# Kernel optimization log

Measured on AMD Instinct MI355X. Metric: run time of the kernel, lower is better.

The kernel has to match this reference:

```python
import jax, jax.numpy as jnp
import numpy as np
import math

N, K, M = 4, 3, 3
OUTC, INC = 64, 64

def _valid_combos():
    combos = []
    for n in range(1, N + 1):
        for k in range(K):
            for m in range(-M, M + 1):
                if abs(m) <= k and k < n:
                    combos.append((n, k, m))
    return combos

COMBOS = _valid_combos()  # 23 (n,k,m) triples, static


def _assoc_laguerre(k, a, x):
    # L_k^a(x) = sum_{i=0}^k (-1)^i C(k+a, k-i) x^i / i!  (static small degree)
    out = jnp.zeros_like(x)
    for i in range(k + 1):
        c = ((-1) ** i) * math.comb(k + a, k - i) / math.factorial(i)
        out = out + jnp.asarray(c, x.dtype) * x ** i
    return out


def _assoc_legendre(l, m, ct, st):
    # P_l^m(cos t) with Condon-Shortley phase; ct=cos t, st=sin t >= 0
    if m > 0:
        dfact = math.prod(range(1, 2 * m, 2))  # (2m-1)!!
        pmm = jnp.asarray(((-1) ** m) * dfact, ct.dtype) * st ** m
    else:
        pmm = jnp.ones_like(ct)
    if l == m:
        return pmm
    pmmp1 = ct * (2 * m + 1) * pmm
    if l == m + 1:
        return pmmp1
    for ll in range(m + 2, l + 1):
        pll = ((2 * ll - 1) * ct * pmmp1 - (ll + m - 1) * pmm) / (ll - m)
        pmm, pmmp1 = pmmp1, pll
    return pmmp1


def _hwfr(n, l, m, r, ct, st, phi):
    # real hydrogen-like wavefunction psi_{n,l,m}(r,theta,phi), a0 = 1
    rho = 2.0 * r / n
    norm_r = math.sqrt((2.0 / n) ** 3 * math.factorial(n - l - 1) / (2 * n * math.factorial(n + l)))
    R = norm_r * jnp.exp(-0.5 * rho) * rho ** l * _assoc_laguerre(n - l - 1, 2 * l + 1, rho)
    am = abs(m)
    Klm = math.sqrt((2 * l + 1) / (4 * math.pi) * math.factorial(l - am) / math.factorial(l + am))
    P = _assoc_legendre(l, am, ct, st)
    if m > 0:
        Y = math.sqrt(2.0) * Klm * jnp.cos(am * phi) * P
    elif m < 0:
        Y = math.sqrt(2.0) * Klm * jnp.sin(am * phi) * P
    else:
        Y = Klm * P
    return R * Y


def setup_inputs() -> dict:
    key = jax.random.key(0)
    k1, k2 = jax.random.split(key)
    position = jax.random.normal(k1, (8, 4096, 3), dtype=jnp.float32)
    coefficients = jax.random.normal(k2, (OUTC, INC, len(COMBOS)), dtype=jnp.float32)
    return {"position": position, "coefficients": coefficients}


def reference(position, coefficients):
    x, y, z = position[..., 0], position[..., 1], position[..., 2]
    r = jnp.sqrt(x * x + y * y + z * z) + 1e-12
    ct = z / r
    st = jnp.sqrt(jnp.clip(1.0 - ct * ct, 0.0, None))
    phi = jnp.arctan2(y, x)
    # (B, P, n_basis) -- loop over the small static basis set, not data dims
    poly = jnp.stack([_hwfr(n, l, m, r, ct, st, phi) for (n, l, m) in COMBOS], axis=-1)
    # einsum 'ijk, mnk -> mnij' as in the torch module -> (OutC, InC, B, P)
    return jnp.einsum('ijk,mnk->mnij', poly, coefficients)
```

## Files before the change

### kernel.cpp

```cpp
#include <hip/hip_runtime.h>
#include <math.h>

#define NPTS  32768
#define NPAIR 4096
#define NC    23
#define TPB   256
#define PPT   4
#define PTS_PER_BLOCK (TPB * PPT)
#define PT    64
#define NCP   24

namespace cgen {
constexpr double PI = 3.14159265358979323846264338327950288;
constexpr double fact(int n) { double r = 1; for (int i = 2; i <= n; ++i) r *= i; return r; }
constexpr double comb(int n, int k) { double r = 1; for (int i = 0; i < k; ++i) r = r * (n - i) / (i + 1); return r; }
constexpr double csqrt(double x) { double g = x > 1 ? x : 1.0; for (int i = 0; i < 100; ++i) g = 0.5 * (g + x / g); return g; }

struct Tables {
  int n[NC]; int l[NC]; int m[NC];
  double pref[NC];
  double lag[NC][4];
};
constexpr Tables gen() {
  Tables t{};
  int idx = 0;
  for (int n = 1; n <= 4; ++n)
    for (int k = 0; k < 3; ++k)
      for (int m = -3; m <= 3; ++m) {
        int am = m < 0 ? -m : m;
        if (!(am <= k && k < n)) continue;
        t.n[idx] = n; t.l[idx] = k; t.m[idx] = m;
        double norm_r = csqrt((2.0 / n) * (2.0 / n) * (2.0 / n) * fact(n - k - 1) / (2.0 * n * fact(n + k)));
        double Klm = csqrt((2.0 * k + 1.0) / (4.0 * PI) * fact(k - am) / fact(k + am));
        t.pref[idx] = norm_r * Klm * (m != 0 ? csqrt(2.0) : 1.0);
        int kk = n - k - 1, a = 2 * k + 1;
        for (int i = 0; i < 4; ++i) t.lag[idx][i] = 0.0;
        for (int i = 0; i <= kk; ++i)
          t.lag[idx][i] = ((i & 1) ? -1.0 : 1.0) * comb(kk + a, kk - i) / fact(i);
        ++idx;
      }
  return t;
}
constexpr Tables T = gen();
}

__global__ __launch_bounds__(TPB)
void dcconv_poly_einsum(const float* __restrict__ pos,
                        const float* __restrict__ coef,
                        float* __restrict__ out) {
  __shared__ __align__(16) float lc[PT * NCP];

  const int tid   = threadIdx.x;
  const int pt0   = blockIdx.x * PTS_PER_BLOCK + tid * PPT;
  const int pair0 = blockIdx.y * PT;

  {
    const float* __restrict__ cb = coef + (size_t)pair0 * NC;
#pragma unroll
    for (int i = tid; i < PT * NC; i += TPB) {
      const int row = i / NC;
      const int col = i - row * NC;
      lc[row * NCP + col] = cb[i];
    }
    if (tid < PT) lc[tid * NCP + NC] = 0.0f;
  }

  const float4* __restrict__ pv = reinterpret_cast<const float4*>(pos + (size_t)pt0 * 3);
  const float4 q0 = pv[0], q1 = pv[1], q2 = pv[2];

  float p0[NC], p1[NC], p2[NC], p3[NC];

  auto evalpt = [&](float x, float y, float z, float (&pc)[NC]) {
    const float r   = sqrtf(x * x + y * y + z * z) + 1e-12f;
    const float ct  = z / r;
    const float st2 = fmaxf(1.0f - ct * ct, 0.0f);
    const float st  = sqrtf(st2);
    const float phi = atan2f(y, x);
    float sp, cp;
    sincosf(phi, &sp, &cp);
    const float c2p = cp * cp - sp * sp;
    const float s2p = 2.0f * sp * cp;

    float rho[5]; rho[0] = 0.0f; rho[1] = 2.0f * r; rho[2] = r; rho[3] = (2.0f / 3.0f) * r; rho[4] = 0.5f * r;
    float en[5];  en[0] = 0.0f;
    en[1] = expf(-r); en[2] = expf(-0.5f * r); en[3] = expf(-(1.0f / 3.0f) * r); en[4] = expf(-0.25f * r);

    float P[3][3] = {};
    P[0][0] = 1.0f;
    P[1][0] = ct;                    P[1][1] = -st;
    P[2][0] = 1.5f * ct * ct - 0.5f; P[2][1] = -3.0f * ct * st; P[2][2] = 3.0f * st2;

    float trig[5]; trig[0] = s2p; trig[1] = sp; trig[2] = 1.0f; trig[3] = cp; trig[4] = c2p;

#pragma unroll
    for (int c = 0; c < NC; ++c) {
      const int n = cgen::T.n[c], l = cgen::T.l[c], m = cgen::T.m[c];
      const int am = m < 0 ? -m : m;
      const float rh = rho[n];
      const float L = (float)cgen::T.lag[c][0]
                    + rh * ((float)cgen::T.lag[c][1]
                    + rh * ((float)cgen::T.lag[c][2]
                    + rh *  (float)cgen::T.lag[c][3]));
      const float rl = (l == 0) ? 1.0f : ((l == 1) ? rh : rh * rh);
      pc[c] = (float)cgen::T.pref[c] * en[n] * rl * L * P[l][am] * trig[m + 2];
    }
  };

  evalpt(q0.x, q0.y, q0.z, p0);
  evalpt(q0.w, q1.x, q1.y, p1);
  evalpt(q1.z, q1.w, q2.x, p2);
  evalpt(q2.y, q2.z, q2.w, p3);

  __syncthreads();

  const float4* __restrict__ lrow = reinterpret_cast<const float4*>(lc);
  float* __restrict__ optr = out + (size_t)pair0 * NPTS + pt0;

#define G4(CV, B)                                                                      \
  a0 = fmaf(CV.x, p0[(B)+0], a0); a1 = fmaf(CV.x, p1[(B)+0], a1);                       \
  a2 = fmaf(CV.x, p2[(B)+0], a2); a3 = fmaf(CV.x, p3[(B)+0], a3);                       \
  a0 = fmaf(CV.y, p0[(B)+1], a0); a1 = fmaf(CV.y, p1[(B)+1], a1);                       \
  a2 = fmaf(CV.y, p2[(B)+1], a2); a3 = fmaf(CV.y, p3[(B)+1], a3);                       \
  a0 = fmaf(CV.z, p0[(B)+2], a0); a1 = fmaf(CV.z, p1[(B)+2], a1);                       \
  a2 = fmaf(CV.z, p2[(B)+2], a2); a3 = fmaf(CV.z, p3[(B)+2], a3);                       \
  a0 = fmaf(CV.w, p0[(B)+3], a0); a1 = fmaf(CV.w, p1[(B)+3], a1);                       \
  a2 = fmaf(CV.w, p2[(B)+3], a2); a3 = fmaf(CV.w, p3[(B)+3], a3);

#define G3(CV, B)                                                                      \
  a0 = fmaf(CV.x, p0[(B)+0], a0); a1 = fmaf(CV.x, p1[(B)+0], a1);                       \
  a2 = fmaf(CV.x, p2[(B)+0], a2); a3 = fmaf(CV.x, p3[(B)+0], a3);                       \
  a0 = fmaf(CV.y, p0[(B)+1], a0); a1 = fmaf(CV.y, p1[(B)+1], a1);                       \
  a2 = fmaf(CV.y, p2[(B)+1], a2); a3 = fmaf(CV.y, p3[(B)+1], a3);                       \
  a0 = fmaf(CV.z, p0[(B)+2], a0); a1 = fmaf(CV.z, p1[(B)+2], a1);                       \
  a2 = fmaf(CV.z, p2[(B)+2], a2); a3 = fmaf(CV.z, p3[(B)+2], a3);

#pragma unroll 2
  for (int j = 0; j < PT; ++j) {
    const float4 c0 = lrow[0], c1 = lrow[1], c2 = lrow[2],
                 c3 = lrow[3], c4 = lrow[4], c5 = lrow[5];
    lrow += 6;

    float a0 = 0.0f, a1 = 0.0f, a2 = 0.0f, a3 = 0.0f;
    G4(c0, 0) G4(c1, 4) G4(c2, 8) G4(c3, 12) G4(c4, 16) G3(c5, 20)

    *reinterpret_cast<float4*>(optr) = make_float4(a0, a1, a2, a3);
    optr += NPTS;
  }
#undef G4
#undef G3
}

extern "C" void kernel_launch(void* const* d_in, const int* in_sizes, int n_in,
                              void* d_out, int out_size, void* d_ws, size_t ws_size,
                              hipStream_t stream) {
  const float* pos  = (const float*)d_in[0];
  const float* coef = (const float*)d_in[1];
  float* out = (float*)d_out;

  dim3 grid(NPTS / PTS_PER_BLOCK, NPAIR / PT);
  dim3 block(TPB);
  hipLaunchKernelGGL(dcconv_poly_einsum, grid, block, 0, stream, pos, coef, out);
}
```

Baseline: 546.7 us.

## Halve points per thread, raise occupancy, simplify trig/exp, prefetch coefficient rows

Result: no change. 540.1 us (-1.2%).

```diff
diff --git a/kernel.cpp b/kernel.cpp
--- a/kernel.cpp
+++ b/kernel.cpp
@@ -5,7 +5,7 @@
 #define NPAIR 4096
 #define NC    23
 #define TPB   256
-#define PPT   4
+#define PPT   2
 #define PTS_PER_BLOCK (TPB * PPT)
 #define PT    64
 #define NCP   24
@@ -44,11 +44,11 @@
 constexpr Tables T = gen();
 }
 
-__global__ __launch_bounds__(TPB)
+__global__ __launch_bounds__(TPB, 4)
 void dcconv_poly_einsum(const float* __restrict__ pos,
                         const float* __restrict__ coef,
                         float* __restrict__ out) {
-  __shared__ __align__(16) float lc[PT * NCP];
+  __shared__ __align__(16) float lc[(PT + 1) * NCP];
 
   const int tid   = threadIdx.x;
   const int pt0   = blockIdx.x * PTS_PER_BLOCK + tid * PPT;
@@ -62,28 +62,31 @@
       const int col = i - row * NC;
       lc[row * NCP + col] = cb[i];
     }
-    if (tid < PT) lc[tid * NCP + NC] = 0.0f;
   }
 
-  const float4* __restrict__ pv = reinterpret_cast<const float4*>(pos + (size_t)pt0 * 3);
-  const float4 q0 = pv[0], q1 = pv[1], q2 = pv[2];
+  const float2* __restrict__ pv = reinterpret_cast<const float2*>(pos + (size_t)pt0 * 3);
+  const float2 f0 = pv[0], f1 = pv[1], f2 = pv[2];
 
-  float p0[NC], p1[NC], p2[NC], p3[NC];
+  float p0[NC], p1[NC];
 
   auto evalpt = [&](float x, float y, float z, float (&pc)[NC]) {
-    const float r   = sqrtf(x * x + y * y + z * z) + 1e-12f;
-    const float ct  = z / r;
-    const float st2 = fmaxf(1.0f - ct * ct, 0.0f);
-    const float st  = sqrtf(st2);
-    const float phi = atan2f(y, x);
-    float sp, cp;
-    sincosf(phi, &sp, &cp);
-    const float c2p = cp * cp - sp * sp;
-    const float s2p = 2.0f * sp * cp;
+    const float rxy2 = x * x + y * y;
+    const float r    = sqrtf(rxy2 + z * z) + 1e-12f;
+    const float ct   = z / r;
+    const float st   = sqrtf(rxy2) / r;
+    const float st2  = st * st;
+    const float invq = rsqrtf(fmaxf(rxy2, 1e-30f));
+    const float cp   = x * invq;
+    const float sp   = y * invq;
+    const float c2p  = (cp - sp) * (cp + sp);
+    const float s2p  = 2.0f * sp * cp;
 
     float rho[5]; rho[0] = 0.0f; rho[1] = 2.0f * r; rho[2] = r; rho[3] = (2.0f / 3.0f) * r; rho[4] = 0.5f * r;
     float en[5];  en[0] = 0.0f;
-    en[1] = expf(-r); en[2] = expf(-0.5f * r); en[3] = expf(-(1.0f / 3.0f) * r); en[4] = expf(-0.25f * r);
+    en[4] = expf(-0.25f * r);
+    en[2] = en[4] * en[4];
+    en[1] = en[2] * en[2];
+    en[3] = expf(-(1.0f / 3.0f) * r);
 
     float P[3][3] = {};
     P[0][0] = 1.0f;
@@ -106,45 +109,42 @@
     }
   };
 
-  evalpt(q0.x, q0.y, q0.z, p0);
-  evalpt(q0.w, q1.x, q1.y, p1);
-  evalpt(q1.z, q1.w, q2.x, p2);
-  evalpt(q2.y, q2.z, q2.w, p3);
+  evalpt(f0.x, f0.y, f1.x, p0);
+  evalpt(f1.y, f2.x, f2.y, p1);
 
   __syncthreads();
 
   const float4* __restrict__ lrow = reinterpret_cast<const float4*>(lc);
   float* __restrict__ optr = out + (size_t)pair0 * NPTS + pt0;
 
-#define G4(CV, B)                                                                      \
-  a0 = fmaf(CV.x, p0[(B)+0], a0); a1 = fmaf(CV.x, p1[(B)+0], a1);                       \
-  a2 = fmaf(CV.x, p2[(B)+0], a2); a3 = fmaf(CV.x, p3[(B)+0], a3);                       \
-  a0 = fmaf(CV.y, p0[(B)+1], a0); a1 = fmaf(CV.y, p1[(B)+1], a1);                       \
-  a2 = fmaf(CV.y, p2[(B)+1], a2); a3 = fmaf(CV.y, p3[(B)+1], a3);                       \
-  a0 = fmaf(CV.z, p0[(B)+2], a0); a1 = fmaf(CV.z, p1[(B)+2], a1);                       \
-  a2 = fmaf(CV.z, p2[(B)+2], a2); a3 = fmaf(CV.z, p3[(B)+2], a3);                       \
-  a0 = fmaf(CV.w, p0[(B)+3], a0); a1 = fmaf(CV.w, p1[(B)+3], a1);                       \
-  a2 = fmaf(CV.w, p2[(B)+3], a2); a3 = fmaf(CV.w, p3[(B)+3], a3);
+#define G4(CV, B)                                                  \
+  a0 = fmaf(CV.x, p0[(B)+0], a0); a1 = fmaf(CV.x, p1[(B)+0], a1);  \
+  a0 = fmaf(CV.y, p0[(B)+1], a0); a1 = fmaf(CV.y, p1[(B)+1], a1);  \
+  a0 = fmaf(CV.z, p0[(B)+2], a0); a1 = fmaf(CV.z, p1[(B)+2], a1);  \
+  a0 = fmaf(CV.w, p0[(B)+3], a0); a1 = fmaf(CV.w, p1[(B)+3], a1);
 
-#define G3(CV, B)                                                                      \
-  a0 = fmaf(CV.x, p0[(B)+0], a0); a1 = fmaf(CV.x, p1[(B)+0], a1);                       \
-  a2 = fmaf(CV.x, p2[(B)+0], a2); a3 = fmaf(CV.x, p3[(B)+0], a3);                       \
-  a0 = fmaf(CV.y, p0[(B)+1], a0); a1 = fmaf(CV.y, p1[(B)+1], a1);                       \
-  a2 = fmaf(CV.y, p2[(B)+1], a2); a3 = fmaf(CV.y, p3[(B)+1], a3);                       \
-  a0 = fmaf(CV.z, p0[(B)+2], a0); a1 = fmaf(CV.z, p1[(B)+2], a1);                       \
-  a2 = fmaf(CV.z, p2[(B)+2], a2); a3 = fmaf(CV.z, p3[(B)+2], a3);
+#define G3(CV, B)                                                  \
+  a0 = fmaf(CV.x, p0[(B)+0], a0); a1 = fmaf(CV.x, p1[(B)+0], a1);  \
+  a0 = fmaf(CV.y, p0[(B)+1], a0); a1 = fmaf(CV.y, p1[(B)+1], a1);  \
+  a0 = fmaf(CV.z, p0[(B)+2], a0); a1 = fmaf(CV.z, p1[(B)+2], a1);
 
-#pragma unroll 2
+  float4 c0 = lrow[0], c1 = lrow[1], c2 = lrow[2],
+         c3 = lrow[3], c4 = lrow[4], c5 = lrow[5];
+
+#pragma unroll 4
   for (int j = 0; j < PT; ++j) {
-    const float4 c0 = lrow[0], c1 = lrow[1], c2 = lrow[2],
-                 c3 = lrow[3], c4 = lrow[4], c5 = lrow[5];
-    lrow += 6;
+    const float4* nrow = lrow + 6 * (j + 1);
+    const float4 n0 = nrow[0], n1 = nrow[1], n2 = nrow[2],
+                 n3 = nrow[3], n4 = nrow[4], n5 = nrow[5];
 
-    float a0 = 0.0f, a1 = 0.0f, a2 = 0.0f, a3 = 0.0f;
+    float a0 = 0.0f, a1 = 0.0f;
     G4(c0, 0) G4(c1, 4) G4(c2, 8) G4(c3, 12) G4(c4, 16) G3(c5, 20)
 
-    *reinterpret_cast<float4*>(optr) = make_float4(a0, a1, a2, a3);
+    float2 res; res.x = a0; res.y = a1;
+    *reinterpret_cast<float2*>(optr) = res;
     optr += NPTS;
+
+    c0 = n0; c1 = n1; c2 = n2; c3 = n3; c4 = n4; c5 = n5;
   }
 #undef G4
 #undef G3
```
